# Kernel tuning notes

Hardware: AMD Instinct MI355X
Metric: run time of the kernel (lower is better)

## Reference

```python
import jax, jax.numpy as jnp
import numpy as np


def setup_inputs() -> dict:
    key = jax.random.key(0)
    k1, k2, k3, k4, k5 = jax.random.split(key, 5)
    x = jax.random.normal(k1, (32, 256, 56, 56), dtype=jnp.float32)
    q_weight = jax.random.randint(k2, (256, 256, 3, 3), 0, 256, dtype=jnp.int32)
    w_scale = jax.random.uniform(k3, (), dtype=jnp.float32) * 0.01 + 1e-4
    w_min = -jax.random.uniform(k4, (), dtype=jnp.float32)
    bias = jax.random.normal(k5, (256,), dtype=jnp.float32)
    return {"x": x, "q_weight": q_weight, "w_scale": w_scale, "w_min": w_min, "bias": bias}


def reference(x, q_weight, w_scale, w_min, bias):
    # Dequantize: affine min/scale scheme -> w = q * scale + min
    w = q_weight.astype(jnp.float32) * w_scale + w_min  # [O, I, kh, kw]
    out = jax.lax.conv_general_dilated(
        x, w,
        window_strides=(1, 1),
        padding=((1, 1), (1, 1)),
        lhs_dilation=(1, 1),
        rhs_dilation=(1, 1),  # dilation=1
        dimension_numbers=("NCHW", "OIHW", "NCHW"),
        feature_group_count=1,  # groups=1
    )
    return out + bias[None, :, None, None]
```

## Files before the change

kernel.cpp:

```cpp
#include <hip/hip_runtime.h>
#include <hip/hip_bf16.h>


typedef __bf16 bf16x8 __attribute__((ext_vector_type(8)));
typedef float floatx4 __attribute__((ext_vector_type(4)));

#define XT_ELEMS 25690112L

__global__ void dequant_w(const int* __restrict__ q, const float* __restrict__ sp,
                          const float* __restrict__ mp, __hip_bfloat16* __restrict__ w2) {
  int g = blockIdx.x * 256 + threadIdx.x;
  float s = sp[0], m = mp[0];
  const int* qp = q + (long)g * 9;
#pragma unroll
  for (int j = 0; j < 9; j++) {
    float w = (float)qp[j] * s + m;
    w2[(long)j * 65536 + g] = __float2bfloat16(w);
  }
}

__global__ __launch_bounds__(256) void transpose_x(const float* __restrict__ x,
                                                   __hip_bfloat16* __restrict__ xt) {
  int n = blockIdx.y;
  int pb = blockIdx.x << 6;
  int t = threadIdx.x;
  int c0 = (t & 63) << 2;
  int p0 = (t >> 6) << 4;

  const float* src = x + (long)n * 802816 + pb;
  __hip_bfloat16* dst = xt + ((long)(n * 3136 + pb)) * 256;

#pragma unroll
  for (int pi = 0; pi < 4; pi++) {
    int p = p0 + pi * 4;
    float v[4][4];
#pragma unroll
    for (int cj = 0; cj < 4; cj++)
      *(float4*)v[cj] = *(const float4*)(src + (long)(c0 + cj) * 3136 + p);
#pragma unroll
    for (int j = 0; j < 4; j++) {
      union {
        ushort4 u;
        __hip_bfloat16 h[4];
      } r;
#pragma unroll
      for (int cj = 0; cj < 4; cj++) r.h[cj] = __float2bfloat16(v[cj][j]);
      *(ushort4*)(dst + (long)(p + j) * 256 + c0) = r.u;
    }
  }
}

__global__ __launch_bounds__(256, 2) void conv_mfma(
    const __hip_bfloat16* __restrict__ xt, const __hip_bfloat16* __restrict__ w2,
    const float* __restrict__ bias, float* __restrict__ out) {
  __shared__ __align__(16) __hip_bfloat16 xs[6 * 58 * 40];
  __shared__ __align__(16) __hip_bfloat16 wsh[3 * 128 * 40];

  int ob = blockIdx.x;
  int rb = blockIdx.y;
  int n = blockIdx.z;
  int t = threadIdx.x;
  int lane = t & 63;
  int wid = t >> 6;
  int wo = (wid & 1) << 6;
  int wpx = (wid >> 1) * 112;
  int l15 = lane & 15, quad = lane >> 4;
  int o0 = ob << 7;
  int h0 = rb << 2;

  int baddr[7];
#pragma unroll
  for (int tt = 0; tt < 7; tt++) {
    int px = wpx + tt * 16 + l15;
    int r = px / 56, c = px - r * 56;
    baddr[tt] = (r * 58 + c) * 40 + quad * 8;
  }

  int xlds[6];
  int xgo[6];
#pragma unroll
  for (int it = 0; it < 6; it++) {
    int q = t + it * 256;
    xlds[it] = -1;
    xgo[it] = -1;
    if (q < 1392) {
      int pos = q >> 2, ck = q & 3;
      int row = pos / 58, col = pos - row * 58;
      int h = h0 - 1 + row, w = col - 1;
      bool v = (h >= 0) && (h < 56) && (w >= 0) && (w < 56);
      xlds[it] = pos * 40 + ck * 8;
      if (v) xgo[it] = (n * 3136 + h * 56 + w) * 256 + ck * 8;
    }
  }

#pragma unroll
  for (int it = 0; it < 6; it++)
    if (xlds[it] >= 0 && xgo[it] < 0) *(int4*)((void*)(xs + xlds[it])) = (int4){0, 0, 0, 0};

  floatx4 acc[4][7];
#pragma unroll
  for (int m = 0; m < 4; m++)
#pragma unroll
    for (int tt = 0; tt < 7; tt++) acc[m][tt] = (floatx4){0.f, 0.f, 0.f, 0.f};

  for (int ib = 0; ib < 8; ib++) {
    int i0 = ib * 32;
    for (int kh = 0; kh < 3; kh++) {
      __syncthreads();
      if (kh == 0) {
#pragma unroll
        for (int it = 0; it < 6; it++)
          if (xgo[it] >= 0)
            *(int4*)((void*)(xs + xlds[it])) = *(const int4*)((const void*)(xt + xgo[it] + i0));
      }
#pragma unroll
      for (int it = 0; it < 6; it++) {
        int q2 = t + it * 256;
        int tap = q2 >> 9;
        int rem = q2 & 511;
        int o_r = rem >> 2, ck = rem & 3;
        int4 v = *(const int4*)((const void*)(
            w2 + ((long)(kh * 3 + tap) * 256 + o0 + o_r) * 256 + i0 + ck * 8));
        *(int4*)((void*)(wsh + (tap * 128 + o_r) * 40 + ck * 8)) = v;
      }
      __syncthreads();

#pragma unroll
      for (int kw = 0; kw < 3; kw++) {
        int koff = (kh * 58 + kw) * 40;
        bf16x8 a[4];
#pragma unroll
        for (int m = 0; m < 4; m++)
          a[m] = *(const bf16x8*)((const void*)(wsh + (kw * 128 + wo + m * 16 + l15) * 40 + quad * 8));
#pragma unroll
        for (int tt = 0; tt < 7; tt++) {
          bf16x8 b = *(const bf16x8*)((const void*)(xs + baddr[tt] + koff));
#pragma unroll
          for (int m = 0; m < 4; m++)
            acc[m][tt] = __builtin_amdgcn_mfma_f32_16x16x32_bf16(a[m], b, acc[m][tt], 0, 0, 0);
        }
      }
    }
  }

#pragma unroll
  for (int m = 0; m < 4; m++) {
    int obase = o0 + wo + m * 16 + quad * 4;
#pragma unroll
    for (int r = 0; r < 4; r++) {
      int o = obase + r;
      float bv = bias[o];
      int outb = (n * 256 + o) * 3136 + h0 * 56;
#pragma unroll
      for (int tt = 0; tt < 7; tt++) {
        int px = wpx + tt * 16 + l15;
        out[outb + px] = acc[m][tt][r] + bv;
      }
    }
  }
}

extern "C" void kernel_launch(void* const* d_in, const int* in_sizes, int n_in,
                              void* d_out, int out_size, void* d_ws, size_t ws_size,
                              hipStream_t stream) {
  const float* x = (const float*)d_in[0];
  const int* qw = (const int*)d_in[1];
  const float* wscale = (const float*)d_in[2];
  const float* wmin = (const float*)d_in[3];
  const float* bias = (const float*)d_in[4];
  float* out = (float*)d_out;

  __hip_bfloat16* xt = (__hip_bfloat16*)d_ws;
  __hip_bfloat16* w2 = (__hip_bfloat16*)((char*)d_ws + XT_ELEMS * 2);

  dequant_w<<<256, 256, 0, stream>>>(qw, wscale, wmin, w2);
  transpose_x<<<dim3(49, 32), 256, 0, stream>>>(x, xt);
  conv_mfma<<<dim3(2, 14, 32), 256, 0, stream>>>(xt, w2, bias, out);
}
```

Baseline: 316.8 us.

## Prefetch next weight/input tiles into registers to overlap global loads with MFMA

```diff
diff --git a/kernel.cpp b/kernel.cpp
--- a/kernel.cpp
+++ b/kernel.cpp
@@ -27,26 +27,26 @@
   int c0 = (t & 63) << 2;
   int p0 = (t >> 6) << 4;
 
-  const float* src = x + (long)n * 802816 + pb;
-  __hip_bfloat16* dst = xt + ((long)(n * 3136 + pb)) * 256;
-
-#pragma unroll
-  for (int pi = 0; pi < 4; pi++) {
-    int p = p0 + pi * 4;
-    float v[4][4];
-#pragma unroll
-    for (int cj = 0; cj < 4; cj++)
-      *(float4*)v[cj] = *(const float4*)(src + (long)(c0 + cj) * 3136 + p);
-#pragma unroll
-    for (int j = 0; j < 4; j++) {
-      union {
-        ushort4 u;
-        __hip_bfloat16 h[4];
-      } r;
-#pragma unroll
-      for (int cj = 0; cj < 4; cj++) r.h[cj] = __float2bfloat16(v[cj][j]);
-      *(ushort4*)(dst + (long)(p + j) * 256 + c0) = r.u;
-    }
+  const float* src = x + (long)n * 802816 + pb + p0;
+  __hip_bfloat16* dst = xt + ((long)(n * 3136 + pb + p0)) * 256 + c0;
+
+  float v[4][16];
+#pragma unroll
+  for (int cj = 0; cj < 4; cj++) {
+    const float* s = src + (long)(c0 + cj) * 3136;
+#pragma unroll
+    for (int pi = 0; pi < 4; pi++)
+      *(float4*)&v[cj][pi * 4] = *(const float4*)(s + pi * 4);
+  }
+#pragma unroll
+  for (int j = 0; j < 16; j++) {
+    union {
+      ushort4 u;
+      __hip_bfloat16 h[4];
+    } r;
+#pragma unroll
+    for (int cj = 0; cj < 4; cj++) r.h[cj] = __float2bfloat16(v[cj][j]);
+    *(ushort4*)(dst + (long)j * 256) = r.u;
   }
 }
 
@@ -93,6 +93,25 @@
     }
   }
 
+  int wlds[6], wbase[6];
+#pragma unroll
+  for (int it = 0; it < 6; it++) {
+    int q2 = t + it * 256;
+    int tap = q2 >> 9;
+    int rem = q2 & 511;
+    int o_r = rem >> 2, ck = rem & 3;
+    wlds[it] = (tap * 128 + o_r) * 40 + ck * 8;
+    wbase[it] = (tap * 256 + o0 + o_r) * 256 + ck * 8;
+  }
+
+  int4 wreg[6], xreg[6];
+#pragma unroll
+  for (int it = 0; it < 6; it++)
+    wreg[it] = *(const int4*)((const void*)(w2 + wbase[it]));
+#pragma unroll
+  for (int it = 0; it < 6; it++)
+    if (xgo[it] >= 0) xreg[it] = *(const int4*)((const void*)(xt + xgo[it]));
+
 #pragma unroll
   for (int it = 0; it < 6; it++)
     if (xlds[it] >= 0 && xgo[it] < 0) *(int4*)((void*)(xs + xlds[it])) = (int4){0, 0, 0, 0};
@@ -104,26 +123,32 @@
     for (int tt = 0; tt < 7; tt++) acc[m][tt] = (floatx4){0.f, 0.f, 0.f, 0.f};
 
   for (int ib = 0; ib < 8; ib++) {
-    int i0 = ib * 32;
     for (int kh = 0; kh < 3; kh++) {
       __syncthreads();
       if (kh == 0) {
 #pragma unroll
         for (int it = 0; it < 6; it++)
-          if (xgo[it] >= 0)
-            *(int4*)((void*)(xs + xlds[it])) = *(const int4*)((const void*)(xt + xgo[it] + i0));
-      }
-#pragma unroll
-      for (int it = 0; it < 6; it++) {
-        int q2 = t + it * 256;
-        int tap = q2 >> 9;
-        int rem = q2 & 511;
-        int o_r = rem >> 2, ck = rem & 3;
-        int4 v = *(const int4*)((const void*)(
-            w2 + ((long)(kh * 3 + tap) * 256 + o0 + o_r) * 256 + i0 + ck * 8));
-        *(int4*)((void*)(wsh + (tap * 128 + o_r) * 40 + ck * 8)) = v;
-      }
+          if (xgo[it] >= 0) *(int4*)((void*)(xs + xlds[it])) = xreg[it];
+      }
+#pragma unroll
+      for (int it = 0; it < 6; it++)
+        *(int4*)((void*)(wsh + wlds[it])) = wreg[it];
       __syncthreads();
+
+      int nib = (kh == 2) ? ib + 1 : ib;
+      int nkh = (kh == 2) ? 0 : kh + 1;
+      if (nib < 8) {
+        int noff = nkh * 196608 + nib * 32;
+#pragma unroll
+        for (int it = 0; it < 6; it++)
+          wreg[it] = *(const int4*)((const void*)(w2 + wbase[it] + noff));
+        if (nkh == 0) {
+          int ni0 = nib * 32;
+#pragma unroll
+          for (int it = 0; it < 6; it++)
+            if (xgo[it] >= 0) xreg[it] = *(const int4*)((const void*)(xt + xgo[it] + ni0));
+        }
+      }
 
 #pragma unroll
       for (int kw = 0; kw < 3; kw++) {
```

Result: slower. 475.9 us (+50.2%).

## Stage transpose through LDS and prefetch conv tiles into registers before barrier

Applied to the files above, without the earlier changes.

```diff
diff --git a/kernel.cpp b/kernel.cpp
--- a/kernel.cpp
+++ b/kernel.cpp
@@ -21,33 +21,38 @@
 
 __global__ __launch_bounds__(256) void transpose_x(const float* __restrict__ x,
                                                    __hip_bfloat16* __restrict__ xt) {
-  int n = blockIdx.y;
+  __shared__ __align__(16) ushort lds[64 * 72];
+  int n = blockIdx.z;
   int pb = blockIdx.x << 6;
+  int cb = blockIdx.y << 6;
   int t = threadIdx.x;
-  int c0 = (t & 63) << 2;
-  int p0 = (t >> 6) << 4;
+  int px0 = (t & 15) << 2;
+  int c0 = (t >> 4) << 2;
 
-  const float* src = x + (long)n * 802816 + pb;
-  __hip_bfloat16* dst = xt + ((long)(n * 3136 + pb)) * 256;
+  const float* src = x + (long)n * 802816 + (long)(cb + c0) * 3136 + pb + px0;
+  float v[4][4];
+#pragma unroll
+  for (int cj = 0; cj < 4; cj++)
+    *(float4*)v[cj] = *(const float4*)(src + (long)cj * 3136);
 
 #pragma unroll
-  for (int pi = 0; pi < 4; pi++) {
-    int p = p0 + pi * 4;
-    float v[4][4];
+  for (int j = 0; j < 4; j++) {
+    int jj = (j + t) & 3;
+    union {
+      ushort4 u;
+      __hip_bfloat16 h[4];
+    } r;
 #pragma unroll
-    for (int cj = 0; cj < 4; cj++)
-      *(float4*)v[cj] = *(const float4*)(src + (long)(c0 + cj) * 3136 + p);
-#pragma unroll
-    for (int j = 0; j < 4; j++) {
-      union {
-        ushort4 u;
-        __hip_bfloat16 h[4];
-      } r;
-#pragma unroll
-      for (int cj = 0; cj < 4; cj++) r.h[cj] = __float2bfloat16(v[cj][j]);
-      *(ushort4*)(dst + (long)(p + j) * 256 + c0) = r.u;
-    }
+    for (int cj = 0; cj < 4; cj++) r.h[cj] = __float2bfloat16(v[cj][jj]);
+    *(ushort4*)&lds[(px0 + jj) * 72 + c0] = r.u;
   }
+  __syncthreads();
+
+  int px = t >> 2;
+  int c8 = (t & 3) << 3;
+  __hip_bfloat16* dst = xt + ((long)(n * 3136 + pb + px)) * 256 + cb;
+  *(int4*)((void*)(dst + c8)) = *(const int4*)((const void*)&lds[px * 72 + c8]);
+  *(int4*)((void*)(dst + c8 + 32)) = *(const int4*)((const void*)&lds[px * 72 + c8 + 32]);
 }
 
 __global__ __launch_bounds__(256, 2) void conv_mfma(
@@ -93,6 +98,17 @@
     }
   }
 
+  int wlds[6], wbase[6];
+#pragma unroll
+  for (int it = 0; it < 6; it++) {
+    int q2 = t + it * 256;
+    int tap = q2 >> 9;
+    int rem = q2 & 511;
+    int o_r = rem >> 2, ck = rem & 3;
+    wlds[it] = (tap * 128 + o_r) * 40 + ck * 8;
+    wbase[it] = (tap * 256 + o0 + o_r) * 256 + ck * 8;
+  }
+
 #pragma unroll
   for (int it = 0; it < 6; it++)
     if (xlds[it] >= 0 && xgo[it] < 0) *(int4*)((void*)(xs + xlds[it])) = (int4){0, 0, 0, 0};
@@ -106,23 +122,26 @@
   for (int ib = 0; ib < 8; ib++) {
     int i0 = ib * 32;
     for (int kh = 0; kh < 3; kh++) {
+      int4 wreg[6], xreg[6];
+      int woff = kh * 196608 + i0;
+#pragma unroll
+      for (int it = 0; it < 6; it++)
+        wreg[it] = *(const int4*)((const void*)(w2 + wbase[it] + woff));
+      if (kh == 0) {
+#pragma unroll
+        for (int it = 0; it < 6; it++)
+          if (xgo[it] >= 0) xreg[it] = *(const int4*)((const void*)(xt + xgo[it] + i0));
+      }
+
       __syncthreads();
       if (kh == 0) {
 #pragma unroll
         for (int it = 0; it < 6; it++)
-          if (xgo[it] >= 0)
-            *(int4*)((void*)(xs + xlds[it])) = *(const int4*)((const void*)(xt + xgo[it] + i0));
+          if (xgo[it] >= 0) *(int4*)((void*)(xs + xlds[it])) = xreg[it];
       }
 #pragma unroll
-      for (int it = 0; it < 6; it++) {
-        int q2 = t + it * 256;
-        int tap = q2 >> 9;
-        int rem = q2 & 511;
-        int o_r = rem >> 2, ck = rem & 3;
-        int4 v = *(const int4*)((const void*)(
-            w2 + ((long)(kh * 3 + tap) * 256 + o0 + o_r) * 256 + i0 + ck * 8));
-        *(int4*)((void*)(wsh + (tap * 128 + o_r) * 40 + ck * 8)) = v;
-      }
+      for (int it = 0; it < 6; it++)
+        *(int4*)((void*)(wsh + wlds[it])) = wreg[it];
       __syncthreads();
 
 #pragma unroll
@@ -174,6 +193,6 @@
   __hip_bfloat16* w2 = (__hip_bfloat16*)((char*)d_ws + XT_ELEMS * 2);
 
   dequant_w<<<256, 256, 0, stream>>>(qw, wscale, wmin, w2);
-  transpose_x<<<dim3(49, 32), 256, 0, stream>>>(x, xt);
+  transpose_x<<<dim3(49, 4, 32), 256, 0, stream>>>(x, xt);
   conv_mfma<<<dim3(2, 14, 32), 256, 0, stream>>>(xt, w2, bias, out);
 }
```

Result: slower. 462.4 us (+46.0%).
